# Performance work log

Hardware: AMD Instinct MI355X
Metric: run time of the kernel (lower is better)

## Reference

```python
import jax, jax.numpy as jnp
import numpy as np
from functools import partial

B, T, I, H = 64, 1024, 256, 256


def _lstm_dir(x_tbi, w_ih, w_hh, b_ih, b_hh, reverse):
    """Coupled-gate LSTM over time. x_tbi: [T,B,I]. Returns hs [T,B,H], (hT, cT).

    Gates = x@W_ih^T + b_ih + h@W_hh^T + b_hh, split into (in, cell, out);
    forget = 1 - in (coupled input/forget gates).
    """
    Bn = x_tbi.shape[1]
    Hn = w_hh.shape[1]
    # Precompute input contribution for all timesteps in one big GEMM.
    gx = jnp.einsum('tbi,gi->tbg', x_tbi, w_ih) + (b_ih + b_hh)  # [T,B,3H]

    def step(carry, g):
        h, c = carry
        gates = g + h @ w_hh.T  # [B,3H]
        ig, cg, og = jnp.split(gates, 3, axis=1)
        ig = jax.nn.sigmoid(ig)
        fg = 1.0 - ig
        cg = jnp.tanh(cg)
        og = jax.nn.sigmoid(og)
        c = fg * c + ig * cg
        h = og * jnp.tanh(c)
        return (h, c), h

    h0 = jnp.zeros((Bn, Hn), dtype=x_tbi.dtype)
    c0 = jnp.zeros((Bn, Hn), dtype=x_tbi.dtype)
    # lax.scan(reverse=True) runs backward in time but stacks outputs in
    # original time order, matching ReverseLSTMLayer's reverse(outputs).
    (hT, cT), hs = jax.lax.scan(step, (h0, c0), gx, reverse=reverse)
    return hs, hT, cT


def setup_inputs() -> dict:
    key = jax.random.key(0)
    ks = jax.random.split(key, 9)
    s = 0.05  # small init scale for numerical sanity
    return {
        'X': jax.random.normal(ks[0], (B, T, I), dtype=jnp.float32),
        'wih_f': jax.random.normal(ks[1], (3 * H, I), dtype=jnp.float32) * s,
        'whh_f': jax.random.normal(ks[2], (3 * H, H), dtype=jnp.float32) * s,
        'bih_f': jax.random.normal(ks[3], (3 * H,), dtype=jnp.float32) * s,
        'bhh_f': jax.random.normal(ks[4], (3 * H,), dtype=jnp.float32) * s,
        'wih_b': jax.random.normal(ks[5], (3 * H, I), dtype=jnp.float32) * s,
        'whh_b': jax.random.normal(ks[6], (3 * H, H), dtype=jnp.float32) * s,
        'bih_b': jax.random.normal(ks[7], (3 * H,), dtype=jnp.float32) * s,
        'bhh_b': jax.random.normal(ks[8], (3 * H,), dtype=jnp.float32) * s,
    }


def reference(X, wih_f, whh_f, bih_f, bhh_f, wih_b, whh_b, bih_b, bhh_b):
    x_tbi = jnp.transpose(X, (1, 0, 2))  # [T,B,I]
    hs_f, hTf, cTf = _lstm_dir(x_tbi, wih_f, whh_f, bih_f, bhh_f, reverse=False)
    hs_b, hTb, cTb = _lstm_dir(x_tbi, wih_b, whh_b, bih_b, bhh_b, reverse=True)
    out = jnp.concatenate([hs_f, hs_b], axis=-1)  # [T,B,2H]
    hn = jnp.concatenate([hTf, hTb], axis=1)[None]  # [1,B,2H]
    cn = jnp.concatenate([cTf, cTb], axis=1)[None]
    return out, hn, cn
```

## Files before the change

kernel.cpp:

```cpp
#include <hip/hip_runtime.h>
#include <cstdint>
#include <cstddef>

#define TT 1024
#define NB 64
#define HD 256
#define NG 768

typedef short bhalf8 __attribute__((ext_vector_type(8)));
typedef float f32x4  __attribute__((ext_vector_type(4)));

#define LOG2E  1.4426950408889634f
#define LOG2E2 2.8853900817779268f

__device__ __forceinline__ float bf2f(unsigned short s) {
  return __uint_as_float(((unsigned)s) << 16);
}
__device__ __forceinline__ unsigned cvt_pk_bf16(float lo, float hi) {
  unsigned r;
  asm("v_cvt_pk_bf16_f32 %0, %1, %2" : "=v"(r) : "v"(lo), "v"(hi));
  return r;
}
__device__ __forceinline__ float clamp24(float x) {
  return __builtin_amdgcn_fmed3f(x, -24.0f, 24.0f);
}
__device__ __forceinline__ void inv4(float d0, float d1, float d2, float d3,
                                     float& i0, float& i1, float& i2, float& i3) {
  float p2 = d0 * d1;
  float p3 = p2 * d2;
  float p4 = p3 * d3;
  float r  = __builtin_amdgcn_rcpf(p4);
  i3 = r * p3;
  float r3 = r * d3;
  i2 = r3 * p2;
  float r2 = r3 * d2;
  i1 = r2 * d0;
  i0 = r2 * d1;
}

#define GX_SLICE ((size_t)TT * NG * 16)

__launch_bounds__(256, 2)
__global__ void gx_kernel(const float* __restrict__ X,
                          const float* __restrict__ wih_f, const float* __restrict__ bih_f,
                          const float* __restrict__ bhh_f,
                          const float* __restrict__ wih_b, const float* __restrict__ bih_b,
                          const float* __restrict__ bhh_b,
                          unsigned short* __restrict__ gx) {
  const int tid = threadIdx.x;
  const int n0  = blockIdx.x * 64;
  const int t0  = blockIdx.y * 4;

  __shared__ unsigned short Al[64][264];
  __shared__ unsigned short Bl[64][264];

  const int lane = tid & 63, w = tid >> 6, quad = lane >> 4, l15 = lane & 15;
  const float wsc = (n0 >= 256 && n0 < 512) ? LOG2E2 : LOG2E;

  for (int dir = 0; dir < 2; ++dir) {
    const float* wih = dir ? wih_b : wih_f;
    const float* bih = dir ? bih_b : bih_f;
    const float* bhh = dir ? bhh_b : bhh_f;
    unsigned short* gxd = gx + (size_t)dir * 4 * GX_SLICE;

    __syncthreads();
#pragma unroll
    for (int i = 0; i < 16; ++i) {
      int f4  = tid + i * 256;
      int row = f4 >> 6;
      int kk  = (f4 & 63) * 4;
      float4 wv = *(const float4*)(wih + (size_t)(n0 + row) * HD + kk);
      uint2 p;
      p.x = cvt_pk_bf16(wv.x * wsc, wv.y * wsc);
      p.y = cvt_pk_bf16(wv.z * wsc, wv.w * wsc);
      *(uint2*)&Bl[row][kk] = p;
    }

    for (int tt = 0; tt < 4; ++tt) {
      const int t = t0 + tt;
      __syncthreads();
#pragma unroll
      for (int i = 0; i < 16; ++i) {
        int f4  = tid + i * 256;
        int row = f4 >> 6;
        int kk  = (f4 & 63) * 4;
        float4 xv = *(const float4*)(X + ((size_t)row * TT + t) * HD + kk);
        uint2 p;
        p.x = cvt_pk_bf16(xv.x, xv.y);
        p.y = cvt_pk_bf16(xv.z, xv.w);
        *(uint2*)&Al[row][kk] = p;
      }
      __syncthreads();

      f32x4 acc[4];
#pragma unroll
      for (int jt = 0; jt < 4; ++jt) { acc[jt][0]=0.f; acc[jt][1]=0.f; acc[jt][2]=0.f; acc[jt][3]=0.f; }

#pragma unroll
      for (int kt = 0; kt < 8; ++kt) {
        bhalf8 a = *(const bhalf8*)&Al[16 * w + l15][kt * 32 + quad * 8];
#pragma unroll
        for (int jt = 0; jt < 4; ++jt) {
          bhalf8 b = *(const bhalf8*)&Bl[jt * 16 + l15][kt * 32 + quad * 8];
          acc[jt] = __builtin_amdgcn_mfma_f32_16x16x32_bf16(a, b, acc[jt], 0, 0, 0);
        }
      }

      unsigned short* gs = gxd + w * GX_SLICE + (size_t)t * NG * 16;
#pragma unroll
      for (int jt = 0; jt < 4; ++jt) {
        int g = n0 + jt * 16 + l15;
        float bias = (bih[g] + bhh[g]) * wsc;
        uint2 p;
        p.x = cvt_pk_bf16(acc[jt][0] + bias, acc[jt][1] + bias);
        p.y = cvt_pk_bf16(acc[jt][2] + bias, acc[jt][3] + bias);
        *(uint2*)(gs + g * 16 + quad * 4) = p;
      }
    }
  }
}

__attribute__((amdgpu_flat_work_group_size(1024, 1024)))
__attribute__((amdgpu_waves_per_eu(4, 4)))
__global__ void rec_kernel(const float* __restrict__ whh_f,
                           const float* __restrict__ whh_b,
                           const unsigned short* __restrict__ gx,
                           float* __restrict__ out) {
  const int tid  = threadIdx.x;
  const int lane = tid & 63, w = tid >> 6, quad = lane >> 4, l15 = lane & 15;
  const int blk = blockIdx.x;
  const int dir = blk >> 2;
  const int b0  = (blk & 3) * 16;
  const float* whh = dir ? whh_b : whh_f;
  const unsigned short* gxd = gx + (size_t)dir * 4 * GX_SLICE + (size_t)(blk & 3) * GX_SLICE;
  float* hn = out + (size_t)TT * NB * 512;
  float* cn = hn + (size_t)NB * 512;

  __shared__ uint4 wlds[16][8][64];
  __shared__ uint4 hk[2][8][64];

  bhalf8 wreg[2][8];
#pragma unroll
  for (int p = 0; p < 3; ++p) {
    int n = p * 256 + 16 * w + l15;
    const float wscp = (p == 1) ? LOG2E2 : LOG2E;
#pragma unroll
    for (int kt = 0; kt < 8; ++kt) {
      const float* wp = whh + (size_t)n * HD + kt * 32 + quad * 8;
      float4 v0 = *(const float4*)wp;
      float4 v1 = *(const float4*)(wp + 4);
      union { bhalf8 v; uint4 u; } pk;
      pk.u.x = cvt_pk_bf16(v0.x * wscp, v0.y * wscp);
      pk.u.y = cvt_pk_bf16(v0.z * wscp, v0.w * wscp);
      pk.u.z = cvt_pk_bf16(v1.x * wscp, v1.y * wscp);
      pk.u.w = cvt_pk_bf16(v1.z * wscp, v1.w * wscp);
      if (p < 2) wreg[p][kt] = pk.v;
      else       wlds[w][kt][lane] = pk.u;
    }
  }

  if (tid < 512) {
    uint4 z; z.x = z.y = z.z = z.w = 0;
    ((uint4*)hk[0])[tid] = z;
  }

  float cstate[4];
#pragma unroll
  for (int r = 0; r < 4; ++r) cstate[r] = 0.0f;

  int goff[3];
#pragma unroll
  for (int p = 0; p < 3; ++p) {
    int g = p * 256 + 16 * w + l15;
    goff[p] = g * 16 + quad * 4;
  }

  __syncthreads();

  const unsigned short* gptr = gxd + (size_t)(dir ? (TT - 1) : 0) * NG * 16;
  const ptrdiff_t gstep = dir ? -(ptrdiff_t)((size_t)NG * 16) : (ptrdiff_t)((size_t)NG * 16);

  float* orow = out + ((size_t)(dir ? (TT - 1) : 0) * NB + b0 + quad * 4) * 512
                + dir * 256 + 16 * w + l15;
  const ptrdiff_t ostep = dir ? -(ptrdiff_t)(NB * 512) : (ptrdiff_t)(NB * 512);

  ushort4 gxv[3];
#pragma unroll
  for (int p = 0; p < 3; ++p) gxv[p] = *(const ushort4*)(gptr + goff[p]);

#pragma unroll 2
  for (int s = 0; s < TT; ++s) {
    const int pb = s & 1;

    f32x4 acc[3];
#pragma unroll
    for (int p = 0; p < 3; ++p) {
      acc[p][0] = bf2f(gxv[p].x); acc[p][1] = bf2f(gxv[p].y);
      acc[p][2] = bf2f(gxv[p].z); acc[p][3] = bf2f(gxv[p].w);
    }
    gptr += gstep;
#pragma unroll
    for (int p = 0; p < 3; ++p) gxv[p] = *(const ushort4*)(gptr + goff[p]);

#pragma unroll
    for (int kt = 0; kt < 8; ++kt) {
      bhalf8 a = __builtin_bit_cast(bhalf8, hk[pb][kt][lane]);
      acc[0] = __builtin_amdgcn_mfma_f32_16x16x32_bf16(a, wreg[0][kt], acc[0], 0, 0, 0);
      acc[1] = __builtin_amdgcn_mfma_f32_16x16x32_bf16(a, wreg[1][kt], acc[1], 0, 0, 0);
      acc[2] = __builtin_amdgcn_mfma_f32_16x16x32_bf16(
          a, __builtin_bit_cast(bhalf8, wlds[w][kt][lane]), acc[2], 0, 0, 0);
    }

    unsigned short* hnext = (unsigned short*)hk[pb ^ 1][w >> 1];
    float ei[4], ec[4], eo[4];
#pragma unroll
    for (int r = 0; r < 4; ++r) {
      ei[r] = __builtin_amdgcn_exp2f(clamp24(-acc[0][r]));
      ec[r] = __builtin_amdgcn_exp2f(clamp24( acc[1][r]));
      eo[r] = __builtin_amdgcn_exp2f(clamp24(-acc[2][r]));
    }
    float ig[4], tc[4], og[4];
    inv4(1.f + ei[0], 1.f + ei[1], 1.f + ei[2], 1.f + ei[3],
         ig[0], ig[1], ig[2], ig[3]);
    inv4(1.f + ec[0], 1.f + ec[1], 1.f + ec[2], 1.f + ec[3],
         tc[0], tc[1], tc[2], tc[3]);
    inv4(1.f + eo[0], 1.f + eo[1], 1.f + eo[2], 1.f + eo[3],
         og[0], og[1], og[2], og[3]);
    float cvv[4], et[4];
#pragma unroll
    for (int r = 0; r < 4; ++r) {
      float cg = __builtin_fmaf(-2.f, tc[r], 1.f);
      float cp = cstate[r];
      float cv = __builtin_fmaf(ig[r], cg - cp, cp);
      cstate[r] = cv;
      cvv[r] = cv;
      et[r] = __builtin_amdgcn_exp2f(cv * LOG2E2);
    }
    float it4[4];
    inv4(1.f + et[0], 1.f + et[1], 1.f + et[2], 1.f + et[3],
         it4[0], it4[1], it4[2], it4[3]);
    float hv[4];
#pragma unroll
    for (int r = 0; r < 4; ++r)
      hv[r] = og[r] * __builtin_fmaf(-2.f, it4[r], 1.f);

    unsigned short* hbj = hnext
        + (size_t)(((((w & 1) * 2 + (l15 >> 3)) * 16) + quad * 4) * 8) + (l15 & 7);
    unsigned u01 = cvt_pk_bf16(hv[0], hv[1]);
    unsigned u23 = cvt_pk_bf16(hv[2], hv[3]);
    hbj[0]  = (unsigned short)u01;
    hbj[8]  = (unsigned short)(u01 >> 16);
    hbj[16] = (unsigned short)u23;
    hbj[24] = (unsigned short)(u23 >> 16);

#pragma unroll
    for (int r = 0; r < 4; ++r) {
      orow[(size_t)r * 512 + 0] = hv[r];
      if (s == TT - 1) {
        int brow = b0 + quad * 4 + r;
        int col  = 16 * w + l15;
        hn[(size_t)brow * 512 + dir * 256 + col] = hv[r];
        cn[(size_t)brow * 512 + dir * 256 + col] = cvv[r];
      }
    }
    orow += ostep;
    __syncthreads();
  }
}

extern "C" void kernel_launch(void* const* d_in, const int* in_sizes, int n_in,
                              void* d_out, int out_size, void* d_ws, size_t ws_size,
                              hipStream_t stream) {
  const float* X     = (const float*)d_in[0];
  const float* wih_f = (const float*)d_in[1];
  const float* whh_f = (const float*)d_in[2];
  const float* bih_f = (const float*)d_in[3];
  const float* bhh_f = (const float*)d_in[4];
  const float* wih_b = (const float*)d_in[5];
  const float* whh_b = (const float*)d_in[6];
  const float* bih_b = (const float*)d_in[7];
  const float* bhh_b = (const float*)d_in[8];
  float* out = (float*)d_out;
  unsigned short* gxbuf = (unsigned short*)d_ws;

  dim3 g1(NG / 64, TT / 4);
  gx_kernel<<<g1, 256, 0, stream>>>(X, wih_f, bih_f, bhh_f, wih_b, bih_b, bhh_b, gxbuf);
  rec_kernel<<<8, 1024, 0, stream>>>(whh_f, whh_b, gxbuf, out);
}
```

Measured before the change: 1.920 ms.

## Restructure input GEMM: register-resident weights, both directions per X tile, double-buffered staging

The input-projection kernel now uses 1024-thread blocks. Each wave keeps its 16-column slice of both directions' W_ih in registers as bf16, so every staged X tile feeds the forward and backward GEMMs together instead of being staged twice. Each block covers 16 timesteps, and the X staging into LDS is double-buffered so the next timestep's load overlaps the current MFMA work, with one barrier per step. This cuts redundant X reloads, LDS weight traffic and synchronisation. The cost is higher register pressure and a smaller grid. The recurrent kernel, which likely dominates total time, is unchanged.

```diff
diff --git a/kernel.cpp b/kernel.cpp
--- a/kernel.cpp
+++ b/kernel.cpp
@@ -40,7 +40,8 @@
 
 #define GX_SLICE ((size_t)TT * NG * 16)
 
-__launch_bounds__(256, 2)
+__attribute__((amdgpu_flat_work_group_size(1024, 1024)))
+__attribute__((amdgpu_waves_per_eu(4, 4)))
 __global__ void gx_kernel(const float* __restrict__ X,
                           const float* __restrict__ wih_f, const float* __restrict__ bih_f,
                           const float* __restrict__ bhh_f,
@@ -49,75 +50,83 @@
                           unsigned short* __restrict__ gx) {
   const int tid = threadIdx.x;
   const int n0  = blockIdx.x * 64;
-  const int t0  = blockIdx.y * 4;
-
-  __shared__ unsigned short Al[64][264];
-  __shared__ unsigned short Bl[64][264];
+  const int t0  = blockIdx.y * 16;
+
+  __shared__ unsigned short Al[2][64][264];
 
   const int lane = tid & 63, w = tid >> 6, quad = lane >> 4, l15 = lane & 15;
+  const int sl = w & 3;
+  const int jt = w >> 2;
+  const int g  = n0 + jt * 16 + l15;
   const float wsc = (n0 >= 256 && n0 < 512) ? LOG2E2 : LOG2E;
 
+  bhalf8 wreg[2][8];
+#pragma unroll
   for (int dir = 0; dir < 2; ++dir) {
     const float* wih = dir ? wih_b : wih_f;
-    const float* bih = dir ? bih_b : bih_f;
-    const float* bhh = dir ? bhh_b : bhh_f;
-    unsigned short* gxd = gx + (size_t)dir * 4 * GX_SLICE;
-
+#pragma unroll
+    for (int kt = 0; kt < 8; ++kt) {
+      const float* wp = wih + (size_t)g * HD + kt * 32 + quad * 8;
+      float4 v0 = *(const float4*)wp;
+      float4 v1 = *(const float4*)(wp + 4);
+      union { bhalf8 v; uint4 u; } pk;
+      pk.u.x = cvt_pk_bf16(v0.x * wsc, v0.y * wsc);
+      pk.u.y = cvt_pk_bf16(v0.z * wsc, v0.w * wsc);
+      pk.u.z = cvt_pk_bf16(v1.x * wsc, v1.y * wsc);
+      pk.u.w = cvt_pk_bf16(v1.z * wsc, v1.w * wsc);
+      wreg[dir][kt] = pk.v;
+    }
+  }
+  const float bias_f = (bih_f[g] + bhh_f[g]) * wsc;
+  const float bias_b = (bih_b[g] + bhh_b[g]) * wsc;
+
+#define STAGE_X(ttv, buf)                                                     \
+  {                                                                           \
+    const int t = t0 + (ttv);                                                 \
+    _Pragma("unroll")                                                         \
+    for (int i = 0; i < 4; ++i) {                                             \
+      int f4  = tid + i * 1024;                                               \
+      int row = f4 >> 6;                                                      \
+      int kk  = (f4 & 63) * 4;                                                \
+      float4 xv = *(const float4*)(X + ((size_t)row * TT + t) * HD + kk);     \
+      uint2 p;                                                                \
+      p.x = cvt_pk_bf16(xv.x, xv.y);                                          \
+      p.y = cvt_pk_bf16(xv.z, xv.w);                                          \
+      *(uint2*)&Al[buf][row][kk] = p;                                         \
+    }                                                                         \
+  }
+
+  STAGE_X(0, 0);
+
+  for (int tt = 0; tt < 16; ++tt) {
+    const int buf = tt & 1;
     __syncthreads();
-#pragma unroll
-    for (int i = 0; i < 16; ++i) {
-      int f4  = tid + i * 256;
-      int row = f4 >> 6;
-      int kk  = (f4 & 63) * 4;
-      float4 wv = *(const float4*)(wih + (size_t)(n0 + row) * HD + kk);
+    if (tt < 15) STAGE_X(tt + 1, buf ^ 1);
+
+    f32x4 acc0 = {0.f, 0.f, 0.f, 0.f};
+    f32x4 acc1 = {0.f, 0.f, 0.f, 0.f};
+#pragma unroll
+    for (int kt = 0; kt < 8; ++kt) {
+      bhalf8 a = *(const bhalf8*)&Al[buf][16 * sl + l15][kt * 32 + quad * 8];
+      acc0 = __builtin_amdgcn_mfma_f32_16x16x32_bf16(a, wreg[0][kt], acc0, 0, 0, 0);
+      acc1 = __builtin_amdgcn_mfma_f32_16x16x32_bf16(a, wreg[1][kt], acc1, 0, 0, 0);
+    }
+
+    const int t = t0 + tt;
+    {
+      unsigned short* gs = gx + sl * GX_SLICE + (size_t)t * NG * 16 + g * 16 + quad * 4;
       uint2 p;
-      p.x = cvt_pk_bf16(wv.x * wsc, wv.y * wsc);
-      p.y = cvt_pk_bf16(wv.z * wsc, wv.w * wsc);
-      *(uint2*)&Bl[row][kk] = p;
-    }
-
-    for (int tt = 0; tt < 4; ++tt) {
-      const int t = t0 + tt;
-      __syncthreads();
-#pragma unroll
-      for (int i = 0; i < 16; ++i) {
-        int f4  = tid + i * 256;
-        int row = f4 >> 6;
-        int kk  = (f4 & 63) * 4;
-        float4 xv = *(const float4*)(X + ((size_t)row * TT + t) * HD + kk);
-        uint2 p;
-        p.x = cvt_pk_bf16(xv.x, xv.y);
-        p.y = cvt_pk_bf16(xv.z, xv.w);
-        *(uint2*)&Al[row][kk] = p;
-      }
-      __syncthreads();
-
-      f32x4 acc[4];
-#pragma unroll
-      for (int jt = 0; jt < 4; ++jt) { acc[jt][0]=0.f; acc[jt][1]=0.f; acc[jt][2]=0.f; acc[jt][3]=0.f; }
-
-#pragma unroll
-      for (int kt = 0; kt < 8; ++kt) {
-        bhalf8 a = *(const bhalf8*)&Al[16 * w + l15][kt * 32 + quad * 8];
-#pragma unroll
-        for (int jt = 0; jt < 4; ++jt) {
-          bhalf8 b = *(const bhalf8*)&Bl[jt * 16 + l15][kt * 32 + quad * 8];
-          acc[jt] = __builtin_amdgcn_mfma_f32_16x16x32_bf16(a, b, acc[jt], 0, 0, 0);
-        }
-      }
-
-      unsigned short* gs = gxd + w * GX_SLICE + (size_t)t * NG * 16;
-#pragma unroll
-      for (int jt = 0; jt < 4; ++jt) {
-        int g = n0 + jt * 16 + l15;
-        float bias = (bih[g] + bhh[g]) * wsc;
-        uint2 p;
-        p.x = cvt_pk_bf16(acc[jt][0] + bias, acc[jt][1] + bias);
-        p.y = cvt_pk_bf16(acc[jt][2] + bias, acc[jt][3] + bias);
-        *(uint2*)(gs + g * 16 + quad * 4) = p;
-      }
-    }
-  }
+      p.x = cvt_pk_bf16(acc0[0] + bias_f, acc0[1] + bias_f);
+      p.y = cvt_pk_bf16(acc0[2] + bias_f, acc0[3] + bias_f);
+      *(uint2*)gs = p;
+      unsigned short* gs1 = gs + 4 * GX_SLICE;
+      uint2 q;
+      q.x = cvt_pk_bf16(acc1[0] + bias_b, acc1[1] + bias_b);
+      q.y = cvt_pk_bf16(acc1[2] + bias_b, acc1[3] + bias_b);
+      *(uint2*)gs1 = q;
+    }
+  }
+#undef STAGE_X
 }
 
 __attribute__((amdgpu_flat_work_group_size(1024, 1024)))
@@ -283,7 +292,7 @@
   float* out = (float*)d_out;
   unsigned short* gxbuf = (unsigned short*)d_ws;
 
-  dim3 g1(NG / 64, TT / 4);
-  gx_kernel<<<g1, 256, 0, stream>>>(X, wih_f, bih_f, bhh_f, wih_b, bih_b, bhh_b, gxbuf);
+  dim3 g1(NG / 64, TT / 16);
+  gx_kernel<<<g1, 1024, 0, stream>>>(X, wih_f, bih_f, bhh_f, wih_b, bih_b, bhh_b, gxbuf);
   rec_kernel<<<8, 1024, 0, stream>>>(whh_f, whh_b, gxbuf, out);
 }
```

Result: no change. 1.898 ms (-1.2%).
